# Performance work log

Hardware: AMD Instinct MI355X
Metric: run time of the kernel (lower is better)

## Reference

```python
import jax, jax.numpy as jnp
import numpy as np
import math

HIDDEN = 768
HEADS = 12
HEAD_DIM = HIDDEN // HEADS  # 64
SEQ = 197
K_RANK = min(128, HEAD_DIM)  # 64
BATCH = 64


def setup_inputs() -> dict:
    key = jax.random.key(0)
    ks = jax.random.split(key, 12)
    init = 0.02
    # Linear weights stored [in, out] (equivalent to torch W.T)
    return {
        "hidden_states": jax.random.normal(ks[0], (BATCH, SEQ, HIDDEN), dtype=jnp.float32),
        "Wq": jax.random.normal(ks[1], (HIDDEN, HIDDEN), dtype=jnp.float32) * init,
        "bq": jnp.zeros((HIDDEN,), dtype=jnp.float32),
        "Wk": jax.random.normal(ks[2], (HIDDEN, HIDDEN), dtype=jnp.float32) * init,
        "bk": jnp.zeros((HIDDEN,), dtype=jnp.float32),
        "Wv": jax.random.normal(ks[3], (HIDDEN, HIDDEN), dtype=jnp.float32) * init,
        "bv": jnp.zeros((HIDDEN,), dtype=jnp.float32),
        "Wo": jax.random.normal(ks[4], (HIDDEN, HIDDEN), dtype=jnp.float32) * init,
        "bo": jnp.zeros((HIDDEN,), dtype=jnp.float32),
        "E_k": jax.random.normal(ks[5], (SEQ, K_RANK), dtype=jnp.float32) * init,
        "E_v": jax.random.normal(ks[6], (SEQ, K_RANK), dtype=jnp.float32) * init,
    }


def reference(hidden_states, Wq, bq, Wk, bk, Wv, bv, Wo, bo, E_k, E_v):
    B, S, D = hidden_states.shape
    H, d = HEADS, HEAD_DIM
    scale = 1.0 / math.sqrt(d)

    def split_heads(x):  # [B,S,D] -> [B,H,S,d]
        return x.reshape(B, S, H, d).transpose(0, 2, 1, 3)

    q = split_heads(hidden_states @ Wq + bq)
    k = split_heads(hidden_states @ Wk + bk)
    v = split_heads(hidden_states @ Wv + bv)

    # low-rank projection of K/V along the sequence axis: [B,H,k,d]
    pk = jnp.einsum('sk,bhsd->bhkd', E_k, k)
    pv = jnp.einsum('sk,bhsd->bhkd', E_v, v)

    # scores over reduced axis: [B,H,S,k]
    scores = jnp.einsum('bhsd,bhkd->bhsk', q, pk) * scale
    probs = jax.nn.softmax(scores, axis=-1)

    ctx = jnp.einsum('bhsk,bhkd->bhsd', probs, pv)
    ctx = ctx.transpose(0, 2, 1, 3).reshape(B, S, D)
    out = ctx @ Wo + bo  # dropout rate 0.0 -> identity
    return out
```

## Files before the change

kernel.cpp:

```cpp
#include <hip/hip_runtime.h>
#include <math.h>

#define B_   64
#define S_   197
#define D_   768
#define H_   12
#define HD_  64
#define M_   (B_ * S_)
#define MPAD 12672
#define KE   224
#define BH_  (B_ * H_)
#define WSZ  ((size_t)D_ * D_)

typedef _Float16 half8_t __attribute__((ext_vector_type(8)));
typedef _Float16 half4_t __attribute__((ext_vector_type(4)));
typedef _Float16 half2_t __attribute__((ext_vector_type(2)));
typedef float floatx4 __attribute__((ext_vector_type(4)));

#define LDS_DMA16(gptr, lptr) \
  __builtin_amdgcn_global_load_lds((const __attribute__((address_space(1))) void*)(gptr), \
                                   (__attribute__((address_space(3))) void*)(lptr), 16, 0, 0)

#define VMCNT(n) do { asm volatile("s_waitcnt vmcnt(" n ")" ::: "memory"); \
                      __builtin_amdgcn_sched_barrier(0); } while (0)
#define BARRIER() do { __builtin_amdgcn_sched_barrier(0); \
                       __builtin_amdgcn_s_barrier(); \
                       __builtin_amdgcn_sched_barrier(0); } while (0)

__global__ __launch_bounds__(256) void prep_y_kernel(
    const float* __restrict__ X,
    const float* __restrict__ Wq, const float* __restrict__ Wk,
    const float* __restrict__ Wv, const float* __restrict__ Wo,
    const float* __restrict__ Ek, const float* __restrict__ Ev,
    _Float16* __restrict__ Xh,
    _Float16* __restrict__ Tcat, _Float16* __restrict__ To,
    float* __restrict__ esumK, float* __restrict__ esumV,
    _Float16* __restrict__ Ybuf)
{
    __shared__ _Float16 smem[KE * 66];
    const int bid = blockIdx.x, tid = threadIdx.x;

    if (bid >= 768 && bid < 3072) {
        const int idx = bid - 768;
        float (*tile)[33] = (float (*)[33])smem;
        const int z = idx / 576, rem = idx % 576;
        const int bx = rem % 24, by = rem / 24;
        const float* W = (z == 0) ? Wk : (z == 1) ? Wv : (z == 2) ? Wq : Wo;
        _Float16* T = (z < 3) ? (Tcat + (size_t)z * WSZ) : To;
        const int n0 = bx * 32, k0 = by * 32;
        const int r = tid >> 3, c4 = (tid & 7) * 4;
        *(float4*)&tile[r][c4] = *(const float4*)&W[(size_t)(k0 + r) * D_ + n0 + c4];
        __syncthreads();
        half4_t o = { (_Float16)tile[c4 + 0][r], (_Float16)tile[c4 + 1][r],
                      (_Float16)tile[c4 + 2][r], (_Float16)tile[c4 + 3][r] };
        *(half4_t*)&T[(size_t)(n0 + r) * D_ + k0 + c4] = o;
        return;
    }

    if (bid >= 3096) {
        const int idx = bid - 3096;
        const float* E = idx ? Ev : Ek;
        float* es = idx ? esumV : esumK;
        if (tid < 64) {
            float acc = 0.f;
            for (int s = 0; s < S_; ++s) acc += E[s * 64 + tid];
            es[tid] = acc;
        }
        return;
    }

    if (bid >= 3072) {
        const int idx = bid - 3072;
        const half8_t z8 = {};
        *(half8_t*)&Xh[(size_t)M_ * D_ + (size_t)(idx * 256 + tid) * 8] = z8;
        return;
    }

    _Float16* Xs = smem;
    const int idx = bid;
    const int b = idx / 12, n0 = (idx % 12) * 64;
    const int w = tid >> 6, lane = tid & 63;
    const int l15 = lane & 15, quad = lane >> 4;

    #pragma unroll
    for (int i = 0; i < 7; ++i) {
        const int s = i * 32 + (tid >> 3);
        const int d0 = (tid & 7) * 8;
        float4 v0 = make_float4(0.f, 0.f, 0.f, 0.f), v1 = v0;
        if (s < S_) {
            const float* src = &X[(size_t)(b * S_ + s) * D_ + n0 + d0];
            v0 = *(const float4*)src;
            v1 = *(const float4*)(src + 4);
        }
        const half8_t h8 = { (_Float16)v0.x, (_Float16)v0.y, (_Float16)v0.z,
                             (_Float16)v0.w, (_Float16)v1.x, (_Float16)v1.y,
                             (_Float16)v1.z, (_Float16)v1.w };
        if (s < S_)
            *(half8_t*)&Xh[(size_t)(b * S_ + s) * D_ + n0 + d0] = h8;
        #pragma unroll
        for (int jj = 0; jj < 4; ++jj) {
            half2_t t2 = { h8[2 * jj], h8[2 * jj + 1] };
            *(half2_t*)&Xs[s * 66 + d0 + 2 * jj] = t2;
        }
    }
    __syncthreads();

    floatx4 acc[2][4] = {};
    #pragma unroll
    for (int k7 = 0; k7 < 7; ++k7) {
        half8_t af[2];
        #pragma unroll
        for (int mi = 0; mi < 2; ++mi) {
            const int row = w * 32 + mi * 16 + l15;
            const float* Esrc = (row < 64) ? Ek : Ev;
            const int er = row & 63;
            #pragma unroll
            for (int jj = 0; jj < 8; ++jj) {
                const int s = k7 * 32 + quad * 8 + jj;
                af[mi][jj] = (_Float16)((s < S_) ? Esrc[s * 64 + er] : 0.f);
            }
        }
        #pragma unroll
        for (int ni = 0; ni < 4; ++ni) {
            const int sb = k7 * 32 + quad * 8;
            half8_t bf;
            #pragma unroll
            for (int jj = 0; jj < 8; ++jj) bf[jj] = Xs[(sb + jj) * 66 + ni * 16 + l15];
            #pragma unroll
            for (int mi = 0; mi < 2; ++mi)
                acc[mi][ni] = __builtin_amdgcn_mfma_f32_16x16x32_f16(
                    af[mi], bf, acc[mi][ni], 0, 0, 0);
        }
    }

    #pragma unroll
    for (int mi = 0; mi < 2; ++mi)
        #pragma unroll
        for (int ni = 0; ni < 4; ++ni)
            #pragma unroll
            for (int i = 0; i < 4; ++i) {
                const int m_local = w * 32 + mi * 16 + quad * 4 + i;
                const int row = (m_local >> 6) * 4096 + b * 64 + (m_local & 63);
                Ybuf[(size_t)row * D_ + n0 + ni * 16 + l15] = (_Float16)acc[mi][ni][i];
            }
}

#define STG32(BUF, T) \
    { _Pragma("unroll") \
      for (int j = 0; j < 2; ++j) { \
          LDS_DMA16(Abase + (size_t)(j * 16) * D_ + (T) * 32, \
                    &sm[(BUF) * 8192 + w * 1024 + j * 512]); \
          LDS_DMA16(Wbase + (size_t)(j * 16) * D_ + (T) * 32, \
                    &sm[(BUF) * 8192 + 4096 + w * 1024 + j * 512]); \
      } }

#define CMP32(BUF) \
    { const int sa = (quad ^ (fr & 3)) * 8; \
      half8_t af[4], bf[4]; \
      _Pragma("unroll") \
      for (int i = 0; i < 4; ++i) { \
          af[i] = *(const half8_t*)&sm[(BUF) * 8192 + (wm + i * 16 + fr) * 32 + sa]; \
          bf[i] = *(const half8_t*)&sm[(BUF) * 8192 + 4096 + (wn + i * 16 + fr) * 32 + sa]; \
      } \
      _Pragma("unroll") \
      for (int mi = 0; mi < 4; ++mi) \
          _Pragma("unroll") \
          for (int ni = 0; ni < 4; ++ni) \
              acc[mi][ni] = __builtin_amdgcn_mfma_f32_16x16x32_f16( \
                  af[mi], bf[ni], acc[mi][ni], 0, 0, 0); }

#define PIPE24() \
    STG32(0, 0); STG32(1, 1); \
    _Pragma("unroll") \
    for (int t = 0; t < 22; ++t) { \
        VMCNT("4"); BARRIER(); \
        STG32((t + 2) % 3, t + 2); \
        CMP32(t % 3); \
    } \
    VMCNT("4"); BARRIER(); \
    CMP32(1); \
    VMCNT("0"); BARRIER(); \
    CMP32(2);

__global__ __launch_bounds__(256) void gemm_qpkv(
    const _Float16* __restrict__ Xh, const _Float16* __restrict__ Ybuf,
    const _Float16* __restrict__ Tcat,
    const float* __restrict__ bq, const float* __restrict__ bk,
    const float* __restrict__ bv,
    const float* __restrict__ esumK, const float* __restrict__ esumV,
    _Float16* __restrict__ Qh, _Float16* __restrict__ pk16,
    _Float16* __restrict__ pvT)
{
    __shared__ _Float16 sm[24576];
    const int bid = blockIdx.x;
    const _Float16 *A, *W;
    const float *bias, *esum;
    _Float16* O16;
    int m0, n0, rowb;
    bool pvt = false;
    if (bid < 624) {
        const int xcd = bid & 7, t = bid >> 3;
        const int slot = t / 6, j = t - slot * 6;
        const int m_blk = slot * 8 + xcd;
        if (m_blk >= MPAD / 128) return;
        m0 = m_blk * 128; n0 = j * 128; rowb = m0;
        A = Xh; W = Tcat + 2 * WSZ + (size_t)n0 * D_;
        bias = bq; esum = nullptr; O16 = Qh;
    } else {
        const int b2 = bid - 624;
        const int xcd = b2 & 7, t = b2 >> 3;
        const int slot = t / 6, j = t - slot * 6;
        const int m_blk = slot * 8 + xcd;
        m0 = m_blk * 128; n0 = j * 128;
        const bool pv = (m_blk >= 32);
        pvt = pv;
        rowb = pv ? m0 - 4096 : m0;
        A = Ybuf; W = Tcat + (pv ? WSZ : 0) + (size_t)n0 * D_;
        bias = pv ? bv : bk; esum = pv ? esumV : esumK;
        O16 = pk16;
    }

    const int tid = threadIdx.x;
    const int w = tid >> 6, lane = tid & 63;
    const int fr = lane & 15, quad = lane >> 4;
    const int l2 = lane >> 2;
    const int c8 = ((lane & 3) ^ (l2 & 3)) * 8;
    const int wm = (w >> 1) * 64, wn = (w & 1) * 64;

    const _Float16* Abase = A + (size_t)(m0 + w * 32 + l2) * D_ + c8;
    const _Float16* Wbase = W + (size_t)(w * 32 + l2) * D_ + c8;

    floatx4 acc[4][4] = {};

    PIPE24();

    float bval[4];
    #pragma unroll
    for (int ni = 0; ni < 4; ++ni)
        bval[ni] = bias[n0 + wn + ni * 16 + fr];

    _Float16* ct = &sm[w * 2176];

    if (pvt) {
        #pragma unroll
        for (int half = 0; half < 2; ++half) {
            #pragma unroll
            for (int ni2 = 0; ni2 < 2; ++ni2) {
                const int ni = half * 2 + ni2;
                #pragma unroll
                for (int mi = 0; mi < 4; ++mi) {
                    const float4 es4 = *(const float4*)&esum[mi * 16 + quad * 4];
                    const float esv[4] = { es4.x, es4.y, es4.z, es4.w };
                    #pragma unroll
                    for (int i = 0; i < 4; ++i)
                        ct[(ni2 * 16 + fr) * 68 + mi * 16 + quad * 4 + i] =
                            (_Float16)(acc[mi][ni][i] + esv[i] * bval[ni]);
                }
            }
            #pragma unroll
            for (int pass = 0; pass < 4; ++pass) {
                const int rr = pass * 8 + (lane >> 3);
                const int cc = (lane & 7) * 8;
                const half8_t v = *(const half8_t*)&ct[rr * 68 + cc];
                *(half8_t*)&pvT[(size_t)(n0 + wn + half * 32 + rr) * 4096
                                + rowb + wm + cc] = v;
            }
        }
        return;
    }

    #pragma unroll
    for (int half = 0; half < 2; ++half) {
        #pragma unroll
        for (int mi2 = 0; mi2 < 2; ++mi2) {
            const int mi = half * 2 + mi2;
            float esv[4] = {1.f, 1.f, 1.f, 1.f};
            if (esum) {
                const float4 es4 = *(const float4*)&esum[mi * 16 + quad * 4];
                esv[0] = es4.x; esv[1] = es4.y; esv[2] = es4.z; esv[3] = es4.w;
            }
            #pragma unroll
            for (int ni = 0; ni < 4; ++ni)
                #pragma unroll
                for (int i = 0; i < 4; ++i)
                    ct[(mi2 * 16 + quad * 4 + i) * 68 + ni * 16 + fr] =
                        (_Float16)(acc[mi][ni][i] + esv[i] * bval[ni]);
        }
        #pragma unroll
        for (int pass = 0; pass < 4; ++pass) {
            const int rr = pass * 8 + (lane >> 3);
            const int cc = (lane & 7) * 8;
            const half8_t v = *(const half8_t*)&ct[rr * 68 + cc];
            *(half8_t*)&O16[(size_t)(rowb + wm + half * 32 + rr) * D_ + n0 + wn + cc] = v;
        }
    }
}

__global__ __launch_bounds__(256) void gemm_o(
    const _Float16* __restrict__ CTX, const _Float16* __restrict__ To,
    const float* __restrict__ bo, float* __restrict__ O32)
{
    __shared__ _Float16 sm[24576];
    const int xcd = blockIdx.x & 7, t = blockIdx.x >> 3;
    const int slot = t / 6, j = t - slot * 6;
    const int m_blk = slot * 8 + xcd;
    if (m_blk >= MPAD / 128) return;
    const int m0 = m_blk * 128, n0 = j * 128;

    const int tid = threadIdx.x;
    const int w = tid >> 6, lane = tid & 63;
    const int fr = lane & 15, quad = lane >> 4;
    const int l2 = lane >> 2;
    const int c8 = ((lane & 3) ^ (l2 & 3)) * 8;
    const int wm = (w >> 1) * 64, wn = (w & 1) * 64;

    const _Float16* Abase = CTX + (size_t)(m0 + w * 32 + l2) * D_ + c8;
    const _Float16* Wbase = To + (size_t)(n0 + w * 32 + l2) * D_ + c8;

    floatx4 acc[4][4] = {};

    PIPE24();

    float bval[4];
    #pragma unroll
    for (int ni = 0; ni < 4; ++ni)
        bval[ni] = bo[n0 + wn + ni * 16 + fr];

    const bool full = (m0 + 128 <= M_);
    #pragma unroll
    for (int ni = 0; ni < 4; ++ni) {
        const int n = n0 + wn + ni * 16 + fr;
        #pragma unroll
        for (int mi = 0; mi < 4; ++mi)
            #pragma unroll
            for (int i = 0; i < 4; ++i) {
                const int m = m0 + wm + mi * 16 + quad * 4 + i;
                if (full || m < M_)
                    O32[(size_t)m * D_ + n] = acc[mi][ni][i] + bval[ni];
            }
    }
}

__global__ __launch_bounds__(256) void attn_kernel(
    const _Float16* __restrict__ Qh, const _Float16* __restrict__ pk16,
    const _Float16* __restrict__ pvT, _Float16* __restrict__ CTXh)
{
    __shared__ _Float16 P[64 * 80];
    const int bh = blockIdx.x, b = bh / H_, h = bh % H_;
    const int tid = threadIdx.x, w = tid >> 6, lane = tid & 63;
    const int l15 = lane & 15, quad = lane >> 4;
    const _Float16* pkB = pk16 + (size_t)(b * 64) * D_ + h * 64;
    const _Float16* pvB = pvT + (size_t)(h * 64) * 4096 + b * 64;
    const size_t qbase = (size_t)(b * S_) * D_ + h * HD_;

    half8_t bkf[4][2], bvf[4][2];
    #pragma unroll
    for (int ni = 0; ni < 4; ++ni)
        #pragma unroll
        for (int kk = 0; kk < 2; ++kk) {
            bkf[ni][kk] = *(const half8_t*)&pkB[(size_t)(ni * 16 + l15) * D_ + kk * 32 + quad * 8];
            bvf[ni][kk] = *(const half8_t*)&pvB[(size_t)(ni * 16 + l15) * 4096 + kk * 32 + quad * 8];
        }

    for (int t = w; t < 13; t += 4) {
        const int srow = t * 16;
        floatx4 acc[4] = {};
        #pragma unroll
        for (int kk = 0; kk < 2; ++kk) {
            const half8_t aq = *(const half8_t*)
                &Qh[qbase + (size_t)(srow + l15) * D_ + kk * 32 + quad * 8];
            #pragma unroll
            for (int ni = 0; ni < 4; ++ni)
                acc[ni] = __builtin_amdgcn_mfma_f32_16x16x32_f16(
                    aq, bkf[ni][kk], acc[ni], 0, 0, 0);
        }
        float p[4][4];
        #pragma unroll
        for (int i = 0; i < 4; ++i) {
            const float s0 = acc[0][i] * 0.125f, s1 = acc[1][i] * 0.125f;
            const float s2 = acc[2][i] * 0.125f, s3 = acc[3][i] * 0.125f;
            float mx = fmaxf(fmaxf(s0, s1), fmaxf(s2, s3));
            #pragma unroll
            for (int off = 1; off < 16; off <<= 1)
                mx = fmaxf(mx, __shfl_xor(mx, off, 64));
            const float e0 = __expf(s0 - mx), e1 = __expf(s1 - mx);
            const float e2 = __expf(s2 - mx), e3 = __expf(s3 - mx);
            float sme = e0 + e1 + e2 + e3;
            #pragma unroll
            for (int off = 1; off < 16; off <<= 1)
                sme += __shfl_xor(sme, off, 64);
            const float inv = 1.f / sme;
            p[0][i] = e0 * inv; p[1][i] = e1 * inv;
            p[2][i] = e2 * inv; p[3][i] = e3 * inv;
        }
        #pragma unroll
        for (int ni = 0; ni < 4; ++ni)
            #pragma unroll
            for (int i = 0; i < 4; ++i)
                P[(w * 16 + quad * 4 + i) * 80 + ni * 16 + l15] = (_Float16)p[ni][i];

        floatx4 accv[4] = {};
        #pragma unroll
        for (int kk = 0; kk < 2; ++kk) {
            const half8_t ap = *(const half8_t*)&P[(w * 16 + l15) * 80 + kk * 32 + quad * 8];
            #pragma unroll
            for (int ni = 0; ni < 4; ++ni)
                accv[ni] = __builtin_amdgcn_mfma_f32_16x16x32_f16(
                    ap, bvf[ni][kk], accv[ni], 0, 0, 0);
        }
        #pragma unroll
        for (int ni = 0; ni < 4; ++ni)
            #pragma unroll
            for (int i = 0; i < 4; ++i) {
                const int s = srow + quad * 4 + i;
                if (s < S_)
                    CTXh[qbase + (size_t)s * D_ + ni * 16 + l15] = (_Float16)accv[ni][i];
            }
    }
}

extern "C" void kernel_launch(void* const* d_in, const int* in_sizes, int n_in,
                              void* d_out, int out_size, void* d_ws, size_t ws_size,
                              hipStream_t stream) {
    const float* X   = (const float*)d_in[0];
    const float* Wq  = (const float*)d_in[1];
    const float* bq  = (const float*)d_in[2];
    const float* Wk  = (const float*)d_in[3];
    const float* bk  = (const float*)d_in[4];
    const float* Wv  = (const float*)d_in[5];
    const float* bv  = (const float*)d_in[6];
    const float* Wo  = (const float*)d_in[7];
    const float* bo  = (const float*)d_in[8];
    const float* E_k = (const float*)d_in[9];
    const float* E_v = (const float*)d_in[10];
    float* out = (float*)d_out;

    char* p = (char*)d_ws;
    _Float16* Xh   = (_Float16*)p; p += (size_t)MPAD * D_ * 2;
    _Float16* Tcat = (_Float16*)p; p += (size_t)3 * WSZ * 2;
    _Float16* To   = (_Float16*)p; p += (size_t)WSZ * 2;
    _Float16* Qh   = (_Float16*)p; p += (size_t)MPAD * D_ * 2;
    float* esumK   = (float*)p;    p += 64 * sizeof(float);
    float* esumV   = (float*)p;    p += 64 * sizeof(float);
    _Float16* Ybuf = (_Float16*)p; p += (size_t)8192 * D_ * 2;
    _Float16* pk16 = (_Float16*)p; p += (size_t)4096 * D_ * 2;
    _Float16* pvT  = (_Float16*)p;

    prep_y_kernel<<<3098, 256, 0, stream>>>(X, Wq, Wk, Wv, Wo, E_k, E_v,
                                            Xh, Tcat, To, esumK, esumV, Ybuf);
    gemm_qpkv<<<1008, 256, 0, stream>>>(Xh, Ybuf, Tcat,
                                        bq, bk, bv, esumK, esumV,
                                        Qh, pk16, pvT);
    attn_kernel<<<BH_, 256, 0, stream>>>(Qh, pk16, pvT, Xh);
    gemm_o<<<624, 256, 0, stream>>>(Xh, To, bo, out);
}
```

Measured before the change: 201.2 us.

## Use 64-wide K double-buffered pipeline in QKV GEMM and raise MFMA priority in attention

```diff
diff --git a/kernel.cpp b/kernel.cpp
--- a/kernel.cpp
+++ b/kernel.cpp
@@ -145,43 +145,6 @@
             }
 }
 
-#define STG32(BUF, T) \
-    { _Pragma("unroll") \
-      for (int j = 0; j < 2; ++j) { \
-          LDS_DMA16(Abase + (size_t)(j * 16) * D_ + (T) * 32, \
-                    &sm[(BUF) * 8192 + w * 1024 + j * 512]); \
-          LDS_DMA16(Wbase + (size_t)(j * 16) * D_ + (T) * 32, \
-                    &sm[(BUF) * 8192 + 4096 + w * 1024 + j * 512]); \
-      } }
-
-#define CMP32(BUF) \
-    { const int sa = (quad ^ (fr & 3)) * 8; \
-      half8_t af[4], bf[4]; \
-      _Pragma("unroll") \
-      for (int i = 0; i < 4; ++i) { \
-          af[i] = *(const half8_t*)&sm[(BUF) * 8192 + (wm + i * 16 + fr) * 32 + sa]; \
-          bf[i] = *(const half8_t*)&sm[(BUF) * 8192 + 4096 + (wn + i * 16 + fr) * 32 + sa]; \
-      } \
-      _Pragma("unroll") \
-      for (int mi = 0; mi < 4; ++mi) \
-          _Pragma("unroll") \
-          for (int ni = 0; ni < 4; ++ni) \
-              acc[mi][ni] = __builtin_amdgcn_mfma_f32_16x16x32_f16( \
-                  af[mi], bf[ni], acc[mi][ni], 0, 0, 0); }
-
-#define PIPE24() \
-    STG32(0, 0); STG32(1, 1); \
-    _Pragma("unroll") \
-    for (int t = 0; t < 22; ++t) { \
-        VMCNT("4"); BARRIER(); \
-        STG32((t + 2) % 3, t + 2); \
-        CMP32(t % 3); \
-    } \
-    VMCNT("4"); BARRIER(); \
-    CMP32(1); \
-    VMCNT("0"); BARRIER(); \
-    CMP32(2);
-
 __global__ __launch_bounds__(256) void gemm_qpkv(
     const _Float16* __restrict__ Xh, const _Float16* __restrict__ Ybuf,
     const _Float16* __restrict__ Tcat,
@@ -191,7 +154,7 @@
     _Float16* __restrict__ Qh, _Float16* __restrict__ pk16,
     _Float16* __restrict__ pvT)
 {
-    __shared__ _Float16 sm[24576];
+    __shared__ _Float16 sm[32768];
     const int bid = blockIdx.x;
     const _Float16 *A, *W;
     const float *bias, *esum;
@@ -222,17 +185,56 @@
 
     const int tid = threadIdx.x;
     const int w = tid >> 6, lane = tid & 63;
-    const int fr = lane & 15, quad = lane >> 4;
-    const int l2 = lane >> 2;
-    const int c8 = ((lane & 3) ^ (l2 & 3)) * 8;
+    const int fr = lane & 15, quad = lane >> 4, f7 = lane & 7;
+    const int l3 = lane >> 3;
+    const int csrc = ((lane & 7) ^ l3) * 8;
     const int wm = (w >> 1) * 64, wn = (w & 1) * 64;
 
-    const _Float16* Abase = A + (size_t)(m0 + w * 32 + l2) * D_ + c8;
-    const _Float16* Wbase = W + (size_t)(w * 32 + l2) * D_ + c8;
+    const _Float16* Abase = A + (size_t)(m0 + w * 32 + l3) * D_ + csrc;
+    const _Float16* Wbase = W + (size_t)(w * 32 + l3) * D_ + csrc;
 
     floatx4 acc[4][4] = {};
 
-    PIPE24();
+#define QPKV_STAGE(BUF, K0) \
+    { _Pragma("unroll") \
+      for (int j = 0; j < 4; ++j) { \
+          LDS_DMA16(Abase + (size_t)(j * 8) * D_ + (K0), &sm[(BUF) * 16384 + w * 2048 + j * 512]); \
+          LDS_DMA16(Wbase + (size_t)(j * 8) * D_ + (K0), &sm[(BUF) * 16384 + 8192 + w * 2048 + j * 512]); \
+      } }
+
+#define QPKV_COMPUTE(BUF) \
+    { _Pragma("unroll") \
+      for (int ksub = 0; ksub < 2; ++ksub) { \
+          const int sa = ((ksub * 4 + quad) ^ f7) * 8; \
+          half8_t af[4], bf[4]; \
+          _Pragma("unroll") \
+          for (int i = 0; i < 4; ++i) { \
+              af[i] = *(const half8_t*)&sm[(BUF) * 16384 + (wm + i * 16 + fr) * 64 + sa]; \
+              bf[i] = *(const half8_t*)&sm[(BUF) * 16384 + 8192 + (wn + i * 16 + fr) * 64 + sa]; \
+          } \
+          _Pragma("unroll") \
+          for (int mi = 0; mi < 4; ++mi) \
+              _Pragma("unroll") \
+              for (int ni = 0; ni < 4; ++ni) \
+                  acc[mi][ni] = __builtin_amdgcn_mfma_f32_16x16x32_f16( \
+                      af[mi], bf[ni], acc[mi][ni], 0, 0, 0); \
+      } }
+
+    QPKV_STAGE(0, 0);
+    __syncthreads();
+    #pragma unroll
+    for (int t = 0; t < 10; t += 2) {
+        QPKV_STAGE(1, (t + 1) * 64);
+        QPKV_COMPUTE(0);
+        __syncthreads();
+        QPKV_STAGE(0, (t + 2) * 64);
+        QPKV_COMPUTE(1);
+        __syncthreads();
+    }
+    QPKV_STAGE(1, 11 * 64);
+    QPKV_COMPUTE(0);
+    __syncthreads();
+    QPKV_COMPUTE(1);
 
     float bval[4];
     #pragma unroll
@@ -296,6 +298,43 @@
     }
 }
 
+#define STG32(BUF, T) \
+    { _Pragma("unroll") \
+      for (int j = 0; j < 2; ++j) { \
+          LDS_DMA16(Abase + (size_t)(j * 16) * D_ + (T) * 32, \
+                    &sm[(BUF) * 8192 + w * 1024 + j * 512]); \
+          LDS_DMA16(Wbase + (size_t)(j * 16) * D_ + (T) * 32, \
+                    &sm[(BUF) * 8192 + 4096 + w * 1024 + j * 512]); \
+      } }
+
+#define CMP32(BUF) \
+    { const int sa = (quad ^ (fr & 3)) * 8; \
+      half8_t af[4], bf[4]; \
+      _Pragma("unroll") \
+      for (int i = 0; i < 4; ++i) { \
+          af[i] = *(const half8_t*)&sm[(BUF) * 8192 + (wm + i * 16 + fr) * 32 + sa]; \
+          bf[i] = *(const half8_t*)&sm[(BUF) * 8192 + 4096 + (wn + i * 16 + fr) * 32 + sa]; \
+      } \
+      _Pragma("unroll") \
+      for (int mi = 0; mi < 4; ++mi) \
+          _Pragma("unroll") \
+          for (int ni = 0; ni < 4; ++ni) \
+              acc[mi][ni] = __builtin_amdgcn_mfma_f32_16x16x32_f16( \
+                  af[mi], bf[ni], acc[mi][ni], 0, 0, 0); }
+
+#define PIPE24() \
+    STG32(0, 0); STG32(1, 1); \
+    _Pragma("unroll") \
+    for (int t = 0; t < 22; ++t) { \
+        VMCNT("4"); BARRIER(); \
+        STG32((t + 2) % 3, t + 2); \
+        CMP32(t % 3); \
+    } \
+    VMCNT("4"); BARRIER(); \
+    CMP32(1); \
+    VMCNT("0"); BARRIER(); \
+    CMP32(2);
+
 __global__ __launch_bounds__(256) void gemm_o(
     const _Float16* __restrict__ CTX, const _Float16* __restrict__ To,
     const float* __restrict__ bo, float* __restrict__ O32)
@@ -365,6 +404,7 @@
     for (int t = w; t < 13; t += 4) {
         const int srow = t * 16;
         floatx4 acc[4] = {};
+        __builtin_amdgcn_s_setprio(1);
         #pragma unroll
         for (int kk = 0; kk < 2; ++kk) {
             const half8_t aq = *(const half8_t*)
@@ -374,6 +414,7 @@
                 acc[ni] = __builtin_amdgcn_mfma_f32_16x16x32_f16(
                     aq, bkf[ni][kk], acc[ni], 0, 0, 0);
         }
+        __builtin_amdgcn_s_setprio(0);
         float p[4][4];
         #pragma unroll
         for (int i = 0; i < 4; ++i) {
@@ -400,6 +441,7 @@
                 P[(w * 16 + quad * 4 + i) * 80 + ni * 16 + l15] = (_Float16)p[ni][i];
 
         floatx4 accv[4] = {};
+        __builtin_amdgcn_s_setprio(1);
         #pragma unroll
         for (int kk = 0; kk < 2; ++kk) {
             const half8_t ap = *(const half8_t*)&P[(w * 16 + l15) * 80 + kk * 32 + quad * 8];
@@ -408,6 +450,7 @@
                 accv[ni] = __builtin_amdgcn_mfma_f32_16x16x32_f16(
                     ap, bvf[ni][kk], accv[ni], 0, 0, 0);
         }
+        __builtin_amdgcn_s_setprio(0);
         #pragma unroll
         for (int ni = 0; ni < 4; ++ni)
             #pragma unroll
```

After: 195.4 us. 2.9% less time.
